# Optimization experiments

Hardware: AMD Instinct MI355X
Metric: run time of the kernel (lower is better)

The kernel has to match this reference:

```python
import jax, jax.numpy as jnp
import numpy as np

N, C, H, W = 8, 256, 128, 128
HW = H * W
NB = 20            # boxes per image
TEMP = 0.5
RATIO = 1.0
IMG_H, IMG_W = 800.0, 800.0  # img_metas[i]['img_shape']


def setup_inputs() -> dict:
    key = jax.random.key(0)
    k1, k2, k3 = jax.random.split(key, 3)
    preds_S = jax.random.normal(k1, (HW, N, C), dtype=jnp.float32)
    preds_T = jax.random.normal(k2, (HW, N, C), dtype=jnp.float32)
    # boxes: random corner pairs in image coords, sorted so x1<=x2, y1<=y2
    u = jax.random.uniform(k3, (N, NB, 4), dtype=jnp.float32)
    x1 = jnp.minimum(u[..., 0], u[..., 2]) * IMG_W
    x2 = jnp.maximum(u[..., 0], u[..., 2]) * IMG_W
    y1 = jnp.minimum(u[..., 1], u[..., 3]) * IMG_H
    y2 = jnp.maximum(u[..., 1], u[..., 3]) * IMG_H
    gt_bboxes = jnp.stack([x1, y1, x2, y2], axis=-1)  # (N, NB, 4)
    return {"preds_S": preds_S, "preds_T": preds_T, "gt_bboxes": gt_bboxes}


def get_attention(preds, temp):
    # preds: (N, C, H, W)
    value = jnp.abs(preds)
    fea_map = value.mean(axis=1)                                   # (N, H, W)
    S_att = (H * W) * jax.nn.softmax((fea_map / temp).reshape(N, -1), axis=1)
    S_att = S_att.reshape(N, H, W)
    channel_map = value.mean(axis=(2, 3))                          # (N, C)
    C_att = C * jax.nn.softmax(channel_map / temp, axis=1)
    return S_att, C_att


def build_masks(gt_bboxes):
    # boxes scaled to feature grid (same math as torch loop, vectorized)
    wmin = jnp.floor(gt_bboxes[..., 0] / IMG_W * W).astype(jnp.int32)  # (N, NB)
    wmax = jnp.ceil(gt_bboxes[..., 2] / IMG_W * W).astype(jnp.int32)
    hmin = jnp.floor(gt_bboxes[..., 1] / IMG_H * H).astype(jnp.int32)
    hmax = jnp.ceil(gt_bboxes[..., 3] / IMG_H * H).astype(jnp.int32)
    area = 1.0 / (hmax + 1 - hmin).astype(jnp.float32) / (wmax + 1 - wmin).astype(jnp.float32)
    hh = jnp.arange(H)[None, None, :, None]
    ww = jnp.arange(W)[None, None, None, :]
    inside = ((hh >= hmin[:, :, None, None]) & (hh <= hmax[:, :, None, None]) &
              (ww >= wmin[:, :, None, None]) & (ww <= wmax[:, :, None, None]))  # (N, NB, H, W)
    # per-box max-scatter == max over boxes of (area where inside else 0)
    Mask_fg = jnp.max(jnp.where(inside, area[:, :, None, None], 0.0), axis=1)  # (N, H, W)
    Mask_bg = (Mask_fg <= 0).astype(jnp.float32)
    s = Mask_bg.sum(axis=(1, 2), keepdims=True)
    Mask_bg = jnp.where(s > 0, Mask_bg / s, Mask_bg)
    return Mask_fg, Mask_bg


def reference(preds_S, preds_T, gt_bboxes):
    # attention from DETACHED teacher features (preds_T.detach() in torch)
    pT_det = jax.lax.stop_gradient(preds_T)
    pT_new = pT_det.reshape(H, W, N, C).transpose(2, 3, 0, 1)  # (N, C, H, W)
    S_t, C_t = get_attention(pT_new, TEMP)

    Mask_fg, Mask_bg = build_masks(gt_bboxes)

    # flatten to the (HW, bs, .) layout of get_fea_loss
    flat = lambda m: m.transpose(1, 2, 0).reshape(HW, N, 1)
    S_t_f = flat(S_t)
    Mfg_f = flat(Mask_fg)
    Mbg_f = flat(Mask_bg)
    C_t_f = C_t[None]  # (1, bs, c) broadcast

    w = jnp.sqrt(S_t_f) * jnp.sqrt(C_t_f)
    fea_t = preds_T * w
    fea_s = preds_S * w
    diff = jnp.abs(fea_s - fea_t)
    fg_loss = jnp.sum(diff * jnp.sqrt(Mfg_f)) / HW
    bg_loss = jnp.sum(diff * jnp.sqrt(Mbg_f)) / HW
    return (fg_loss + bg_loss) * RATIO
```

## Files before the change

kernel.cpp:

```cpp
#include <hip/hip_runtime.h>

#define N_   8
#define C_   256
#define H_   128
#define W_   128
#define HW_  16384
#define NB_  20
constexpr float TEMP  = 0.5f;
constexpr float IMG_W = 800.0f;
constexpr float IMG_H = 800.0f;

__device__ __forceinline__ float waveReduceSum(float v) {
    v += __shfl_xor(v, 32, 64);
    v += __shfl_xor(v, 16, 64);
    v += __shfl_xor(v, 8, 64);
    v += __shfl_xor(v, 4, 64);
    v += __shfl_xor(v, 2, 64);
    v += __shfl_xor(v, 1, 64);
    return v;
}

__global__ __launch_bounds__(256, 4) void k_stats(const float* __restrict__ pT,
                                                  const float* __restrict__ gt,
                                                  float* __restrict__ chan_sum,
                                                  float* __restrict__ fea_sum,
                                                  unsigned int* __restrict__ smax_bits,
                                                  float* __restrict__ Mfg,
                                                  float* __restrict__ bgcnt) {
    const int n     = blockIdx.x & 7;
    const int chunk = blockIdx.x >> 3;
    const int wave  = threadIdx.x >> 6;
    const int lane  = threadIdx.x & 63;
    const int hwb   = chunk * 64;
    const int hw0   = hwb + wave * 16;

    float4 cacc = make_float4(0.f, 0.f, 0.f, 0.f);
    float vmax = 0.f;
    #pragma unroll
    for (int g = 0; g < 4; ++g) {
        const int r = hw0 + g * 4;
        float p[4];
        #pragma unroll
        for (int j = 0; j < 4; ++j) {
            const float4 v = *(const float4*)(pT + ((size_t)((r + j) * N_ + n)) * C_ + lane * 4);
            const float ax = fabsf(v.x), ay = fabsf(v.y), az = fabsf(v.z), aw = fabsf(v.w);
            cacc.x += ax; cacc.y += ay; cacc.z += az; cacc.w += aw;
            p[j] = ax + ay + az + aw;
        }
        float a01 = (lane & 32) ? p[1] : p[0];
        float b01 = (lane & 32) ? p[0] : p[1];
        const float u01 = a01 + __shfl_xor(b01, 32, 64);
        float a23 = (lane & 32) ? p[3] : p[2];
        float b23 = (lane & 32) ? p[2] : p[3];
        const float u23 = a23 + __shfl_xor(b23, 32, 64);
        float aq = (lane & 16) ? u23 : u01;
        float bq = (lane & 16) ? u01 : u23;
        float u = aq + __shfl_xor(bq, 16, 64);
        u += __shfl_xor(u, 8, 64);
        u += __shfl_xor(u, 4, 64);
        u += __shfl_xor(u, 2, 64);
        u += __shfl_xor(u, 1, 64);
        vmax = fmaxf(vmax, u);
        if ((lane & 15) == 0) {
            const int q = lane >> 4;
            const int row = ((q & 1) << 1) | (q >> 1);
            fea_sum[n * HW_ + r + row] = u;
        }
    }
    vmax = fmaxf(vmax, __shfl_xor(vmax, 16, 64));
    vmax = fmaxf(vmax, __shfl_xor(vmax, 32, 64));
    if (lane == 0) atomicMax(&smax_bits[n], __float_as_uint(vmax));

    __shared__ float lds[4][C_];
    ((float4*)lds[wave])[lane] = cacc;
    __syncthreads();
    const int c = threadIdx.x;
    const float cs = lds[0][c] + lds[1][c] + lds[2][c] + lds[3][c];
    atomicAdd(&chan_sum[n * C_ + c], cs);

    if (threadIdx.x < 64) {
        const int hw = hwb + threadIdx.x;
        const int h = hw >> 7, w = hw & 127;
        float fg = 0.f;
        for (int b = 0; b < NB_; ++b) {
            const float* bx = gt + ((size_t)n * NB_ + b) * 4;
            const float x1 = bx[0], y1 = bx[1], x2 = bx[2], y2 = bx[3];
            const int wmin = (int)floorf(x1 / IMG_W * (float)W_);
            const int wmax = (int)ceilf (x2 / IMG_W * (float)W_);
            const int hmin = (int)floorf(y1 / IMG_H * (float)H_);
            const int hmax = (int)ceilf (y2 / IMG_H * (float)H_);
            if (h >= hmin && h <= hmax && w >= wmin && w <= wmax) {
                const float area = 1.0f / (float)(hmax + 1 - hmin) / (float)(wmax + 1 - wmin);
                fg = fmaxf(fg, area);
            }
        }
        Mfg[n * HW_ + hw] = fg;
        const unsigned long long m = __ballot(fg <= 0.f);
        if (threadIdx.x == 0) atomicAdd(&bgcnt[n], (float)__popcll(m));
    }
}

__global__ __launch_bounds__(256) void k_soft(const float* __restrict__ fea_sum,
                                              const float* __restrict__ chan_sum,
                                              const unsigned int* __restrict__ smax_bits,
                                              float* __restrict__ sden_part,
                                              float* __restrict__ B) {
    const int n   = blockIdx.x >> 3;
    const int sub = blockIdx.x & 7;
    const int tid = threadIdx.x;
    __shared__ float red[256];
    const float sm = __uint_as_float(smax_bits[n]) * (1.0f / (C_ * TEMP));
    float acc = 0.f;
    const int base = n * HW_ + sub * 2048;
    #pragma unroll
    for (int k = 0; k < 8; ++k)
        acc += expf(fea_sum[base + k * 256 + tid] * (1.0f / (C_ * TEMP)) - sm);
    red[tid] = acc; __syncthreads();
    for (int s = 128; s > 0; s >>= 1) { if (tid < s) red[tid] += red[tid + s]; __syncthreads(); }
    if (tid == 0) sden_part[blockIdx.x] = red[0];

    if (blockIdx.x >= 8) return;
    __syncthreads();
    const int n2 = blockIdx.x;
    const float lc = chan_sum[n2 * C_ + tid] * (1.0f / (HW_ * TEMP));
    red[tid] = lc; __syncthreads();
    for (int s = 128; s > 0; s >>= 1) { if (tid < s) red[tid] = fmaxf(red[tid], red[tid + s]); __syncthreads(); }
    const float cmax = red[0]; __syncthreads();
    const float e = expf(lc - cmax);
    red[tid] = e; __syncthreads();
    for (int s = 128; s > 0; s >>= 1) { if (tid < s) red[tid] += red[tid + s]; __syncthreads(); }
    B[n2 * C_ + tid] = sqrtf((float)C_ * e / red[0]);
}

__global__ __launch_bounds__(256, 4) void k_main(const float* __restrict__ pS,
                                                 const float* __restrict__ pT,
                                                 const float* __restrict__ fea_sum,
                                                 const float* __restrict__ Mfg,
                                                 const float* __restrict__ bgcnt,
                                                 const unsigned int* __restrict__ smax_bits,
                                                 const float* __restrict__ sden_part,
                                                 const float* __restrict__ B,
                                                 float* __restrict__ partials) {
    const int wave = threadIdx.x >> 6, lane = threadIdx.x & 63;
    const int wg   = blockIdx.x * 4 + wave;
    const int n    = wg & 7;
    const int widx = wg >> 3;
    const int hw0  = widx * 16;
    const float sm = __uint_as_float(smax_bits[n]) * (1.0f / (C_ * TEMP));
    float sden = 0.f;
    #pragma unroll
    for (int j = 0; j < 8; ++j) sden += sden_part[n * 8 + j];
    const float bgs   = bgcnt[n];
    const float bginv = (bgs > 0.f) ? 1.0f / bgs : 1.0f;
    const float4 B4 = *(const float4*)(B + n * C_ + lane * 4);
    float acc = 0.f;
    #pragma unroll 4
    for (int i = 0; i < 16; ++i) {
        const int hw = hw0 + i;
        const float fs = fea_sum[n * HW_ + hw];
        const float fg = Mfg[n * HW_ + hw];
        const float S_att = (float)HW_ * expf(fs * (1.0f / (C_ * TEMP)) - sm) / sden;
        const float bg = (fg <= 0.f) ? bginv : 0.f;
        const float a_row = sqrtf(S_att) * (sqrtf(fg) + sqrtf(bg)) * (1.0f / (float)HW_);
        const size_t off = ((size_t)(hw * N_ + n)) * C_ + lane * 4;
        const float4 sv = *(const float4*)(pS + off);
        const float4 tv = *(const float4*)(pT + off);
        const float part = fabsf(sv.x - tv.x) * B4.x + fabsf(sv.y - tv.y) * B4.y +
                           fabsf(sv.z - tv.z) * B4.z + fabsf(sv.w - tv.w) * B4.w;
        acc += a_row * part;
    }
    acc = waveReduceSum(acc);
    __shared__ float red[4];
    if (lane == 0) red[wave] = acc;
    __syncthreads();
    if (threadIdx.x == 0) partials[blockIdx.x] = red[0] + red[1] + red[2] + red[3];
}

__global__ __launch_bounds__(256) void k_final(const float* __restrict__ partials,
                                               float* __restrict__ out) {
    float a = 0.f;
    for (int i = threadIdx.x; i < 2048; i += 256) a += partials[i];
    __shared__ float red[256];
    red[threadIdx.x] = a; __syncthreads();
    for (int s = 128; s > 0; s >>= 1) { if (threadIdx.x < s) red[threadIdx.x] += red[threadIdx.x + s]; __syncthreads(); }
    if (threadIdx.x == 0) out[0] = red[0];
}

extern "C" void kernel_launch(void* const* d_in, const int* in_sizes, int n_in,
                              void* d_out, int out_size, void* d_ws, size_t ws_size,
                              hipStream_t stream) {
    const float* pS = (const float*)d_in[0];
    const float* pT = (const float*)d_in[1];
    const float* gt = (const float*)d_in[2];
    float* ws = (float*)d_ws;

    float* chan_sum      = ws;
    float* bgcnt         = ws + 2048;
    unsigned int* smax   = (unsigned int*)(ws + 2056);
    float* sden_part     = ws + 2064;
    float* fea_sum       = ws + 4096;
    float* Mfg           = fea_sum + N_ * HW_;
    float* B             = Mfg + N_ * HW_;
    float* partials      = B + N_ * C_;

    hipMemsetAsync(ws, 0, 2064 * sizeof(float), stream);

    k_stats<<<2048, 256, 0, stream>>>(pT, gt, chan_sum, fea_sum, smax, Mfg, bgcnt);
    k_soft <<<64,   256, 0, stream>>>(fea_sum, chan_sum, smax, sden_part, B);
    k_main <<<2048, 256, 0, stream>>>(pS, pT, fea_sum, Mfg, bgcnt, smax, sden_part, B, partials);
    k_final<<<1,    256, 0, stream>>>(partials, (float*)d_out);
}
```

Measured before the change: 390.3 us.

## Replace global atomics and memset with per-block partials; move mask build to k_soft

k_stats no longer issues atomicAdd/atomicMax. Each block writes its per-channel sums and its max to dedicated partial buffers, which k_soft then reduces. The foreground-mask construction and background count also move out of k_stats into k_soft, and the hipMemsetAsync is dropped. This removes contended atomics, one memset launch and divergent box work from the bandwidth-bound stats pass. In exchange it adds a 2 MB partial-sum buffer and a serial 256-step channel reduction in a few k_soft blocks.

```diff
diff --git a/kernel.cpp b/kernel.cpp
--- a/kernel.cpp
+++ b/kernel.cpp
@@ -21,18 +21,14 @@
 }
 
 __global__ __launch_bounds__(256, 4) void k_stats(const float* __restrict__ pT,
-                                                  const float* __restrict__ gt,
-                                                  float* __restrict__ chan_sum,
+                                                  float* __restrict__ chan_part,
                                                   float* __restrict__ fea_sum,
-                                                  unsigned int* __restrict__ smax_bits,
-                                                  float* __restrict__ Mfg,
-                                                  float* __restrict__ bgcnt) {
+                                                  float* __restrict__ smax_part) {
     const int n     = blockIdx.x & 7;
     const int chunk = blockIdx.x >> 3;
     const int wave  = threadIdx.x >> 6;
     const int lane  = threadIdx.x & 63;
-    const int hwb   = chunk * 64;
-    const int hw0   = hwb + wave * 16;
+    const int hw0   = chunk * 64 + wave * 16;
 
     float4 cacc = make_float4(0.f, 0.f, 0.f, 0.f);
     float vmax = 0.f;
@@ -69,47 +65,40 @@
     }
     vmax = fmaxf(vmax, __shfl_xor(vmax, 16, 64));
     vmax = fmaxf(vmax, __shfl_xor(vmax, 32, 64));
-    if (lane == 0) atomicMax(&smax_bits[n], __float_as_uint(vmax));
 
     __shared__ float lds[4][C_];
+    __shared__ float wmax[4];
+    if (lane == 0) wmax[wave] = vmax;
     ((float4*)lds[wave])[lane] = cacc;
     __syncthreads();
     const int c = threadIdx.x;
-    const float cs = lds[0][c] + lds[1][c] + lds[2][c] + lds[3][c];
-    atomicAdd(&chan_sum[n * C_ + c], cs);
-
-    if (threadIdx.x < 64) {
-        const int hw = hwb + threadIdx.x;
-        const int h = hw >> 7, w = hw & 127;
-        float fg = 0.f;
-        for (int b = 0; b < NB_; ++b) {
-            const float* bx = gt + ((size_t)n * NB_ + b) * 4;
-            const float x1 = bx[0], y1 = bx[1], x2 = bx[2], y2 = bx[3];
-            const int wmin = (int)floorf(x1 / IMG_W * (float)W_);
-            const int wmax = (int)ceilf (x2 / IMG_W * (float)W_);
-            const int hmin = (int)floorf(y1 / IMG_H * (float)H_);
-            const int hmax = (int)ceilf (y2 / IMG_H * (float)H_);
-            if (h >= hmin && h <= hmax && w >= wmin && w <= wmax) {
-                const float area = 1.0f / (float)(hmax + 1 - hmin) / (float)(wmax + 1 - wmin);
-                fg = fmaxf(fg, area);
-            }
-        }
-        Mfg[n * HW_ + hw] = fg;
-        const unsigned long long m = __ballot(fg <= 0.f);
-        if (threadIdx.x == 0) atomicAdd(&bgcnt[n], (float)__popcll(m));
-    }
+    chan_part[((size_t)(n * 256 + chunk)) * C_ + c] =
+        lds[0][c] + lds[1][c] + lds[2][c] + lds[3][c];
+    if (threadIdx.x == 0)
+        smax_part[n * 256 + chunk] =
+            fmaxf(fmaxf(wmax[0], wmax[1]), fmaxf(wmax[2], wmax[3]));
 }
 
 __global__ __launch_bounds__(256) void k_soft(const float* __restrict__ fea_sum,
-                                              const float* __restrict__ chan_sum,
-                                              const unsigned int* __restrict__ smax_bits,
+                                              const float* __restrict__ chan_part,
+                                              const float* __restrict__ smax_part,
+                                              const float* __restrict__ gt,
                                               float* __restrict__ sden_part,
+                                              float* __restrict__ bg_part,
+                                              float* __restrict__ Mfg,
+                                              float* __restrict__ stats,
                                               float* __restrict__ B) {
     const int n   = blockIdx.x >> 3;
     const int sub = blockIdx.x & 7;
     const int tid = threadIdx.x;
     __shared__ float red[256];
-    const float sm = __uint_as_float(smax_bits[n]) * (1.0f / (C_ * TEMP));
+
+    red[tid] = smax_part[n * 256 + tid];
+    __syncthreads();
+    for (int s = 128; s > 0; s >>= 1) { if (tid < s) red[tid] = fmaxf(red[tid], red[tid + s]); __syncthreads(); }
+    const float sm = red[0] * (1.0f / (C_ * TEMP));
+    __syncthreads();
+
     float acc = 0.f;
     const int base = n * HW_ + sub * 2048;
     #pragma unroll
@@ -117,27 +106,61 @@
         acc += expf(fea_sum[base + k * 256 + tid] * (1.0f / (C_ * TEMP)) - sm);
     red[tid] = acc; __syncthreads();
     for (int s = 128; s > 0; s >>= 1) { if (tid < s) red[tid] += red[tid + s]; __syncthreads(); }
-    if (tid == 0) sden_part[blockIdx.x] = red[0];
-
-    if (blockIdx.x >= 8) return;
-    __syncthreads();
-    const int n2 = blockIdx.x;
-    const float lc = chan_sum[n2 * C_ + tid] * (1.0f / (HW_ * TEMP));
+    if (tid == 0) sden_part[n * 8 + sub] = red[0];
+    __syncthreads();
+
+    float fg[8] = {0.f, 0.f, 0.f, 0.f, 0.f, 0.f, 0.f, 0.f};
+    for (int b = 0; b < NB_; ++b) {
+        const float* bx = gt + ((size_t)n * NB_ + b) * 4;
+        const float x1 = bx[0], y1 = bx[1], x2 = bx[2], y2 = bx[3];
+        const int wmin = (int)floorf(x1 / IMG_W * (float)W_);
+        const int wmax = (int)ceilf (x2 / IMG_W * (float)W_);
+        const int hmin = (int)floorf(y1 / IMG_H * (float)H_);
+        const int hmax = (int)ceilf (y2 / IMG_H * (float)H_);
+        const float area = 1.0f / (float)(hmax + 1 - hmin) / (float)(wmax + 1 - wmin);
+        #pragma unroll
+        for (int k = 0; k < 8; ++k) {
+            const int hw = sub * 2048 + k * 256 + tid;
+            const int h = hw >> 7, w = hw & 127;
+            if (h >= hmin && h <= hmax && w >= wmin && w <= wmax)
+                fg[k] = fmaxf(fg[k], area);
+        }
+    }
+    float bgc = 0.f;
+    #pragma unroll
+    for (int k = 0; k < 8; ++k) {
+        const int hw = sub * 2048 + k * 256 + tid;
+        Mfg[n * HW_ + hw] = fg[k];
+        bgc += (fg[k] <= 0.f) ? 1.f : 0.f;
+    }
+    red[tid] = bgc; __syncthreads();
+    for (int s = 128; s > 0; s >>= 1) { if (tid < s) red[tid] += red[tid + s]; __syncthreads(); }
+    if (tid == 0) bg_part[n * 8 + sub] = red[0];
+    if (tid == 0 && sub == 0) stats[n] = sm;
+
+    if (sub != 0) return;
+    __syncthreads();
+
+    float cs = 0.f;
+    #pragma unroll 4
+    for (int k2 = 0; k2 < 256; ++k2)
+        cs += chan_part[((size_t)(n * 256 + k2)) * C_ + tid];
+    const float lc = cs * (1.0f / (HW_ * TEMP));
     red[tid] = lc; __syncthreads();
     for (int s = 128; s > 0; s >>= 1) { if (tid < s) red[tid] = fmaxf(red[tid], red[tid + s]); __syncthreads(); }
     const float cmax = red[0]; __syncthreads();
     const float e = expf(lc - cmax);
     red[tid] = e; __syncthreads();
     for (int s = 128; s > 0; s >>= 1) { if (tid < s) red[tid] += red[tid + s]; __syncthreads(); }
-    B[n2 * C_ + tid] = sqrtf((float)C_ * e / red[0]);
+    B[n * C_ + tid] = sqrtf((float)C_ * e / red[0]);
 }
 
 __global__ __launch_bounds__(256, 4) void k_main(const float* __restrict__ pS,
                                                  const float* __restrict__ pT,
                                                  const float* __restrict__ fea_sum,
                                                  const float* __restrict__ Mfg,
-                                                 const float* __restrict__ bgcnt,
-                                                 const unsigned int* __restrict__ smax_bits,
+                                                 const float* __restrict__ bg_part,
+                                                 const float* __restrict__ stats,
                                                  const float* __restrict__ sden_part,
                                                  const float* __restrict__ B,
                                                  float* __restrict__ partials) {
@@ -146,11 +169,10 @@
     const int n    = wg & 7;
     const int widx = wg >> 3;
     const int hw0  = widx * 16;
-    const float sm = __uint_as_float(smax_bits[n]) * (1.0f / (C_ * TEMP));
-    float sden = 0.f;
-    #pragma unroll
-    for (int j = 0; j < 8; ++j) sden += sden_part[n * 8 + j];
-    const float bgs   = bgcnt[n];
+    const float sm = stats[n];
+    float sden = 0.f, bgs = 0.f;
+    #pragma unroll
+    for (int j = 0; j < 8; ++j) { sden += sden_part[n * 8 + j]; bgs += bg_part[n * 8 + j]; }
     const float bginv = (bgs > 0.f) ? 1.0f / bgs : 1.0f;
     const float4 B4 = *(const float4*)(B + n * C_ + lane * 4);
     float acc = 0.f;
@@ -194,19 +216,20 @@
     const float* gt = (const float*)d_in[2];
     float* ws = (float*)d_ws;
 
-    float* chan_sum      = ws;
-    float* bgcnt         = ws + 2048;
-    unsigned int* smax   = (unsigned int*)(ws + 2056);
-    float* sden_part     = ws + 2064;
-    float* fea_sum       = ws + 4096;
-    float* Mfg           = fea_sum + N_ * HW_;
-    float* B             = Mfg + N_ * HW_;
-    float* partials      = B + N_ * C_;
-
-    hipMemsetAsync(ws, 0, 2064 * sizeof(float), stream);
-
-    k_stats<<<2048, 256, 0, stream>>>(pT, gt, chan_sum, fea_sum, smax, Mfg, bgcnt);
-    k_soft <<<64,   256, 0, stream>>>(fea_sum, chan_sum, smax, sden_part, B);
-    k_main <<<2048, 256, 0, stream>>>(pS, pT, fea_sum, Mfg, bgcnt, smax, sden_part, B, partials);
+    float* chan_part = ws;
+    float* smax_part = chan_part + 524288;
+    float* sden_part = smax_part + 2048;
+    float* bg_part   = sden_part + 64;
+    float* stats     = bg_part + 64;
+    float* fea_sum   = ws + 528384;
+    float* Mfg       = fea_sum + N_ * HW_;
+    float* B         = Mfg + N_ * HW_;
+    float* partials  = B + N_ * C_;
+
+    k_stats<<<2048, 256, 0, stream>>>(pT, chan_part, fea_sum, smax_part);
+    k_soft <<<64,   256, 0, stream>>>(fea_sum, chan_part, smax_part, gt,
+                                      sden_part, bg_part, Mfg, stats, B);
+    k_main <<<2048, 256, 0, stream>>>(pS, pT, fea_sum, Mfg, bg_part, stats,
+                                      sden_part, B, partials);
     k_final<<<1,    256, 0, stream>>>(partials, (float*)d_out);
 }
```

After: 315.0 us. 19.3% less time.
